# Kernel tuning notes

Hardware: AMD Instinct MI355X
Metric: run time of the kernel (lower is better)

The kernel has to match this reference:

```python
import jax, jax.numpy as jnp
import numpy as np

WIDTH = 1024
NH = 16
HD = 64
MBS = 16
B = 4
L = 2048
BASE_LR = 1.0
EPS = 1e-6


def gelu_tanh(x):
    return jax.nn.gelu(x, approximate=True)


def gelu_bwd(x):
    t = jnp.tanh(0.79788456 * x * (1 + 0.044715 * x * x))
    return 0.5 * x * ((1 - t * t) * (0.79788456 + 0.1070322243 * x * x)) + 0.5 * (1 + t)


def ln_fwd(x, g, b):
    mu = x.mean(-1, keepdims=True)
    var = ((x - mu) ** 2).mean(-1, keepdims=True)
    return g * ((x - mu) * jax.lax.rsqrt(var + EPS)) + b


def ln_l2_bwd(x, tgt, g, b):
    # grad of 0.5*||LN(x)-tgt||^2 wrt x
    mu = x.mean(-1, keepdims=True)
    var = ((x - mu) ** 2).mean(-1, keepdims=True)
    std = jnp.sqrt(var + EPS)
    xh = (x - mu) / std
    gx = (g * xh + b - tgt) * g
    return (gx - gx.mean(-1, keepdims=True) - xh * (gx * xh).mean(-1, keepdims=True)) / std


def adapter_forward(hidden_states, Wq, Wk, Wv, Wo, Wg, lr_w, lr_b,
                    learnable_token_idx, norm_w, norm_b, W1, b1, W2, b2,
                    post_w, post_b):
    Bb, Ll, width = hidden_states.shape
    nh, hd = norm_w.shape
    mbs = learnable_token_idx.shape[0]
    nc = Ll // mbs  # L chosen divisible by mini_batch_size

    def split_heads(x):  # [B,L,width] -> [B,nh,nc,mbs,hd]
        return x.reshape(Bb, Ll, nh, hd).transpose(0, 2, 1, 3).reshape(Bb, nh, nc, mbs, hd)

    XQ = split_heads(hidden_states @ Wq.T)
    XK = split_heads(hidden_states @ Wk.T)
    XV = split_heads(hidden_states @ Wv.T)

    # eta: learnable per-token lr gate (get_eta)
    X = hidden_states.reshape(Bb, nc, mbs, width)
    lr = jnp.einsum('bnkc,hdc->bhnkd', X, lr_w) + lr_b.reshape(1, nh, 1, 1, 1)
    lr = jax.nn.sigmoid(lr).transpose(0, 1, 2, 4, 3)  # [B,nh,nc,1,mbs]
    lr_eta = BASE_LR * lr / hd
    token_idx = jnp.clip(1.0 / jnp.arange(1, mbs + 1, dtype=hidden_states.dtype)
                         + learnable_token_idx, 0.0, None)
    token_eta = token_idx.reshape(1, 1, 1, mbs, 1)
    eta = token_eta * lr_eta  # [B,nh,nc,mbs,mbs]

    tril = jnp.tril(jnp.ones((mbs, mbs), dtype=hidden_states.dtype))
    lnw = norm_w.reshape(nh, 1, hd)
    lnb = norm_b.reshape(nh, 1, hd)

    def step(carry, xs):
        W1s, b1s, W2s, b2s = carry  # [B,nh,hd,4hd], [B,nh,1,4hd], [B,nh,4hd,hd], [B,nh,1,hd]
        XQm, XKm, XVm, etam = xs    # [B,nh,mbs,hd] x3, [B,nh,mbs,mbs]
        X1 = XKm
        Z1 = X1 @ W1s + b1s
        X2 = gelu_tanh(Z1)
        Z2 = X2 @ W2s + b2s
        gZ2 = ln_l2_bwd(Z2, XVm - XKm, lnw, lnb)
        gZ1 = (gZ2 @ jnp.swapaxes(W2s, -1, -2)) * gelu_bwd(Z1)
        eta_tril = etam * tril
        Attn1 = tril * (XQm @ jnp.swapaxes(X1, -1, -2))
        b1_bar = b1s - eta_tril @ gZ1
        Z1_bar = XQm @ W1s - (etam * Attn1) @ gZ1 + b1_bar
        X2_bar = gelu_tanh(Z1_bar)
        Attn2 = tril * (X2_bar @ jnp.swapaxes(X2, -1, -2))
        b2_bar = b2s - eta_tril @ gZ2
        Z2_bar = X2_bar @ W2s - (etam * Attn2) @ gZ2 + b2_bar
        last = etam[:, :, -1, :, None]  # [B,nh,mbs,1]
        W1n = W1s - jnp.swapaxes(last * X1, -1, -2) @ gZ1
        b1n = b1s - (last * gZ1).sum(-2, keepdims=True)
        W2n = W2s - jnp.swapaxes(last * X2, -1, -2) @ gZ2
        b2n = b2s - (last * gZ2).sum(-2, keepdims=True)
        XQW = XQm + ln_fwd(Z2_bar, lnw, lnb)
        return (W1n, b1n, W2n, b2n), XQW

    carry0 = (jnp.broadcast_to(W1, (Bb,) + W1.shape),
              jnp.broadcast_to(b1, (Bb,) + b1.shape),
              jnp.broadcast_to(W2, (Bb,) + W2.shape),
              jnp.broadcast_to(b2, (Bb,) + b2.shape))
    xs = tuple(jnp.moveaxis(t, 2, 0) for t in (XQ, XK, XV, eta))
    _, XQW = jax.lax.scan(step, carry0, xs)  # [nc,B,nh,mbs,hd]
    out = XQW.transpose(1, 0, 3, 2, 4).reshape(Bb, Ll, width)

    # post_norm (LayerNorm eps=1e-6)
    out = ln_fwd(out, post_w, post_b)
    # gate
    out = gelu_tanh(hidden_states @ Wg.T) * out
    # o_proj
    return out @ Wo.T


def setup_inputs():
    key = jax.random.key(0)
    ks = jax.random.split(key, 10)
    n = lambda k, s: jax.random.normal(k, s, dtype=jnp.float32) * 0.02
    return {
        'hidden_states': jax.random.normal(ks[0], (B, L, WIDTH), dtype=jnp.float32),
        'Wq': n(ks[1], (WIDTH, WIDTH)),
        'Wk': n(ks[2], (WIDTH, WIDTH)),
        'Wv': n(ks[3], (WIDTH, WIDTH)),
        'Wo': n(ks[4], (WIDTH, WIDTH)),
        'Wg': n(ks[5], (WIDTH, WIDTH)),
        'lr_w': n(ks[6], (NH, 1, WIDTH)),
        'lr_b': jnp.zeros((NH, 1), jnp.float32),
        'learnable_token_idx': jnp.zeros((MBS,), jnp.float32),
        'norm_w': jnp.ones((NH, HD), jnp.float32),
        'norm_b': jnp.zeros((NH, HD), jnp.float32),
        'W1': n(ks[7], (NH, HD, 4 * HD)),
        'b1': jnp.zeros((NH, 1, 4 * HD), jnp.float32),
        'W2': n(ks[8], (NH, 4 * HD, HD)),
        'b2': jnp.zeros((NH, 1, HD), jnp.float32),
        'post_w': jnp.ones((WIDTH,), jnp.float32),
        'post_b': jnp.zeros((WIDTH,), jnp.float32),
    }


def reference(hidden_states, Wq, Wk, Wv, Wo, Wg, lr_w, lr_b, learnable_token_idx,
              norm_w, norm_b, W1, b1, W2, b2, post_w, post_b):
    return adapter_forward(hidden_states, Wq, Wk, Wv, Wo, Wg, lr_w, lr_b,
                           learnable_token_idx, norm_w, norm_b, W1, b1, W2, b2,
                           post_w, post_b)
```

## Files before the change

### kernel.cpp

```cpp
#include <hip/hip_runtime.h>

#define WIDTH 1024
#define MBSZ 16
#define LLL 2048
#define NCHUNK 128

typedef __attribute__((ext_vector_type(4))) float f32x4;
typedef __attribute__((ext_vector_type(2))) float f32x2;
typedef __attribute__((ext_vector_type(8))) short short8;
typedef __attribute__((ext_vector_type(4))) short short4v;
typedef __attribute__((ext_vector_type(2))) unsigned u32x2;
typedef __attribute__((ext_vector_type(4))) unsigned u32x4;

#define MFMA16(a, b, c) __builtin_amdgcn_mfma_f32_16x16x32_bf16((a), (b), (c), 0, 0, 0)

__device__ __forceinline__ short f2bf(float f) {
  unsigned u = __float_as_uint(f);
  u = (u + 0x7FFFu + ((u >> 16) & 1u)) >> 16;
  return (short)u;
}
__device__ __forceinline__ float bf2f(short s) {
  return __uint_as_float(((unsigned)(unsigned short)s) << 16);
}
__device__ __forceinline__ unsigned cvt_pk(float lo, float hi) {
  unsigned r;
  asm("v_cvt_pk_bf16_f32 %0, %1, %2" : "=v"(r) : "v"(lo), "v"(hi));
  return r;
}
__device__ __forceinline__ float fast_e2u(float x) {
  return __builtin_amdgcn_exp2f(x * (2.30220776f + 0.10294322f * x * x));
}
__device__ __forceinline__ float gelu_f(float x) {
  float e = fast_e2u(x);
  return x * (1.0f - __builtin_amdgcn_rcpf(e + 1.0f));
}
__device__ __forceinline__ float gelu_bwd_f(float x) {
  float e = fast_e2u(x);
  float r = __builtin_amdgcn_rcpf(e + 1.0f);
  return 2.0f * x * r * (1.0f - r) * (0.79788456f + 0.1070322243f * x * x) + (1.0f - r);
}
__device__ __forceinline__ int w2row(int d) { return d * 264 + (d >> 3) * 24; }

__global__ __launch_bounds__(256) void cvt_kernel(const float* __restrict__ hs,
                                                  const float* __restrict__ Wq,
                                                  const float* __restrict__ Wk,
                                                  const float* __restrict__ Wv,
                                                  const float* __restrict__ Wg,
                                                  const float* __restrict__ Wo,
                                                  short* __restrict__ dst) {
  const long idx = ((long)blockIdx.x * 256 + threadIdx.x) * 8;
  if (idx >= 13631488L) return;
  const float* src;
  long off;
  if (idx < 8388608L)       { src = hs; off = idx; }
  else if (idx < 9437184L)  { src = Wq; off = idx - 8388608L; }
  else if (idx < 10485760L) { src = Wk; off = idx - 9437184L; }
  else if (idx < 11534336L) { src = Wv; off = idx - 10485760L; }
  else if (idx < 12582912L) { src = Wg; off = idx - 11534336L; }
  else                      { src = Wo; off = idx - 12582912L; }
  const f32x4 a = *(const f32x4*)(src + off);
  const f32x4 b = *(const f32x4*)(src + off + 4);
  u32x4 o;
  o[0] = cvt_pk(a[0], a[1]); o[1] = cvt_pk(a[2], a[3]);
  o[2] = cvt_pk(b[0], b[1]); o[3] = cvt_pk(b[2], b[3]);
  *(u32x4*)(dst + idx) = o;
}

template <int OUTBF>
__global__ __launch_bounds__(256) void gemm_bt_b(const short* __restrict__ A,
                                                 const short* __restrict__ W,
                                                 float* __restrict__ C,
                                                 short* __restrict__ Cb) {
  __shared__ __align__(16) short sA[64][40];
  __shared__ __align__(16) short sB[64][40];
  const int tid = threadIdx.x;
  const int m0 = blockIdx.x * 64, n0 = blockIdx.y * 64;
  const int srow = tid >> 2, sk = (tid & 3) * 8;
  const int wv = tid >> 6, ln = tid & 63;
  const int fr = ln & 15, kh = (ln >> 4) * 8;
  f32x4 acc[4];
#pragma unroll
  for (int s = 0; s < 4; ++s) acc[s] = (f32x4){0.f, 0.f, 0.f, 0.f};
  const short* ga = A + (long)(m0 + srow) * 1024 + sk;
  const short* gw = W + (long)(n0 + srow) * 1024 + sk;
  for (int k0 = 0; k0 < 1024; k0 += 32) {
    const short8 a8 = *(const short8*)(ga + k0);
    const short8 w8 = *(const short8*)(gw + k0);
    *(short8*)&sA[srow][sk] = a8;
    *(short8*)&sB[srow][sk] = w8;
    __syncthreads();
    short8 af = *(const short8*)&sA[wv * 16 + fr][kh];
#pragma unroll
    for (int s = 0; s < 4; ++s) {
      short8 bf8 = *(const short8*)&sB[s * 16 + fr][kh];
      acc[s] = MFMA16(af, bf8, acc[s]);
    }
    __syncthreads();
  }
  const int orow = m0 + wv * 16 + (ln >> 4) * 4;
#pragma unroll
  for (int s = 0; s < 4; ++s)
#pragma unroll
    for (int q = 0; q < 4; ++q) {
      if (OUTBF)
        Cb[(long)(orow + q) * 1024 + n0 + s * 16 + fr] = f2bf(acc[s][q]);
      else
        C[(long)(orow + q) * 1024 + n0 + s * 16 + fr] = acc[s][q];
    }
}

__global__ __launch_bounds__(256) void lr_kernel(const float* __restrict__ hs,
                                                 const float* __restrict__ lrw,
                                                 const float* __restrict__ lrb,
                                                 float* __restrict__ out) {
  __shared__ __align__(16) float row[1024];
  const int t = blockIdx.x, tid = threadIdx.x;
  *(f32x4*)&row[tid * 4] = *(const f32x4*)&hs[(long)t * 1024 + tid * 4];
  __syncthreads();
  const int hh = tid >> 4, j = tid & 15;
  const float* wrow = lrw + hh * 1024;
  float s = 0.f;
#pragma unroll 4
  for (int m = 0; m < 16; ++m) {
    const int c = j * 4 + m * 64;
    f32x4 x = *(const f32x4*)&row[c];
    f32x4 w = *(const f32x4*)&wrow[c];
    s += x[0] * w[0] + x[1] * w[1] + x[2] * w[2] + x[3] * w[3];
  }
#pragma unroll
  for (int o = 8; o; o >>= 1) s += __shfl_xor(s, o, 16);
  if (j == 0) {
    const float v = s + lrb[hh];
    const float sg = 1.f / (1.f + expf(-v));
    const int b = t >> 11, tr = t & 2047;
    out[((b << 4) + hh) * 2048 + tr] = sg * (1.f / 64.f);
  }
}

__global__ __launch_bounds__(512, 2) void scan_kernel(
    float* __restrict__ Qb, const float* __restrict__ Kb, const float* __restrict__ Vb,
    const float* __restrict__ LRb, const float* __restrict__ lti,
    const float* __restrict__ nw, const float* __restrict__ nb,
    const float* __restrict__ W1in, const float* __restrict__ b1in,
    const float* __restrict__ W2in, const float* __restrict__ b2in) {
  __shared__ __align__(16) short sW1b[256 * 72];
  __shared__ __align__(16) short sW2dp[64 * 264 + 192];
  __shared__ __align__(16) short la1T[64 * 24];
  __shared__ __align__(16) short la2T[256 * 24];
  __shared__ __align__(16) short sX1b[16 * 72];
  __shared__ __align__(16) short sXQb[16 * 72];
  __shared__ __align__(16) float sXQf[16 * 68];
  __shared__ __align__(16) float sTg[16 * 72];
  __shared__ __align__(16) short sX2b[16 * 264];
  __shared__ __align__(16) short sXbb[16 * 264];
  __shared__ __align__(16) short sG1c[256 * 24];
  __shared__ __align__(16) short sG2b[16 * 72];
  __shared__ __align__(16) short sG2c[64 * 24];
  __shared__ __align__(16) float sZ2f[16 * 68];
  __shared__ __align__(16) short sC1b[16 * 24];
  __shared__ __align__(16) short sC2b[16 * 24];
  __shared__ __align__(16) float sB1[256];
  __shared__ __align__(16) float sB2[64];
  __shared__ float sLr[16];
  __shared__ float sTok[16];
  __shared__ __align__(16) float sLnw[64];
  __shared__ __align__(16) float sLnb[64];

  const int bh = blockIdx.x, b = bh >> 4, h = bh & 15;
  const int tid = threadIdx.x;
  const int w = tid >> 6, ln = tid & 63;
  const int fr = ln & 15, half = ln >> 4, hk = half * 8;
  const int nt0 = 2 * w;

  float w1m[8][4], w2m[8][4];
#pragma unroll
  for (int r = 0; r < 8; ++r) {
    const int T = w * 8 + r, dt = T >> 4, pt = T & 15;
#pragma unroll
    for (int qq = 0; qq < 4; ++qq) {
      w1m[r][qq] = W1in[h * 16384 + (dt * 16 + half * 4 + qq) * 256 + pt * 16 + fr];
      w2m[r][qq] = W2in[h * 16384 + (pt * 16 + half * 4 + qq) * 64 + dt * 16 + fr];
    }
  }
  for (int e = tid; e < 16384; e += 512) {
    {
      const int d = e >> 8, p = e & 255;
      sW1b[p * 72 + d] = f2bf(W1in[h * 16384 + e]);
    }
    {
      const int p = e >> 6, d = e & 63;
      sW2dp[w2row(d) + (p ^ (((d >> 3) & 3) << 3))] = f2bf(W2in[h * 16384 + e]);
    }
  }
  if (tid < 256) sB1[tid] = b1in[h * 256 + tid];
  if (tid < 64) { sB2[tid] = b2in[h * 64 + tid]; sLnw[tid] = nw[h * 64 + tid]; sLnb[tid] = nb[h * 64 + tid]; }
  if (tid < 16) sTok[tid] = fmaxf(1.0f / (float)(tid + 1) + lti[tid], 0.0f);

  const f32x4 zf4 = (f32x4){0.f, 0.f, 0.f, 0.f};
  short8 zs8;
#pragma unroll
  for (int j = 0; j < 8; ++j) zs8[j] = 0;

  const int pf_i = tid >> 5;
  const int pf_d = (tid & 31) * 2;
  f32x2 pk, pq, pv;
  float plr = 0.f;
  {
    const long a0 = ((long)(b * LLL + pf_i)) * WIDTH + h * 64 + pf_d;
    pk = *(const f32x2*)&Kb[a0];
    pq = *(const f32x2*)&Qb[a0];
    pv = *(const f32x2*)&Vb[a0];
    if (tid < 16) plr = LRb[(long)bh * 2048 + tid];
  }

  for (int n = 0; n < NCHUNK; ++n) {
    const long gbase = ((long)(b * LLL + n * MBSZ)) * WIDTH + h * 64;

    {
      *(unsigned*)&sX1b[pf_i * 72 + pf_d] = cvt_pk(pk[0], pk[1]);
      *(unsigned*)&sXQb[pf_i * 72 + pf_d] = cvt_pk(pq[0], pq[1]);
      sXQf[pf_i * 68 + pf_d] = pq[0];
      sXQf[pf_i * 68 + pf_d + 1] = pq[1];
      sTg[pf_i * 72 + pf_d] = pv[0] - pk[0];
      sTg[pf_i * 72 + pf_d + 1] = pv[1] - pk[1];
      if (tid < 16) sLr[tid] = plr;
    }
    __syncthreads();

    short8 aX1[2], aXQ[2];
    aX1[0] = *(const short8*)&sX1b[fr * 72 + hk];
    aX1[1] = *(const short8*)&sX1b[fr * 72 + 32 + hk];
    aXQ[0] = *(const short8*)&sXQb[fr * 72 + hk];
    aXQ[1] = *(const short8*)&sXQb[fr * 72 + 32 + hk];
    f32x4 z1[2], q1[2];
    float b1p[2];
#pragma unroll
    for (int t = 0; t < 2; ++t) {
      const int p = (nt0 + t) * 16 + fr;
      z1[t] = zf4; q1[t] = zf4;
#pragma unroll
      for (int ks = 0; ks < 2; ++ks) {
        short8 bw = *(const short8*)&sW1b[p * 72 + ks * 32 + hk];
        z1[t] = MFMA16(aX1[ks], bw, z1[t]);
        q1[t] = MFMA16(aXQ[ks], bw, q1[t]);
      }
      b1p[t] = sB1[p];
#pragma unroll
      for (int qq = 0; qq < 4; ++qq) {
        z1[t][qq] += b1p[t];
        sX2b[(half * 4 + qq) * 264 + p] = f2bf(gelu_f(z1[t][qq]));
      }
    }
    {
      const float tok15 = sTok[15];
      const int d = tid >> 3, j0 = (tid & 7) * 2;
      const float v0 = bf2f(sX1b[j0 * 72 + d]) * (tok15 * sLr[j0]);
      const float v1 = bf2f(sX1b[(j0 + 1) * 72 + d]) * (tok15 * sLr[j0 + 1]);
      *(unsigned*)&la1T[d * 24 + j0] = cvt_pk(v0, v1);
    }
    if (w == 0) {
      f32x4 c = MFMA16(aXQ[0], aX1[0], zf4);
      c = MFMA16(aXQ[1], aX1[1], c);
#pragma unroll
      for (int qq = 0; qq < 4; ++qq) {
        const int i = half * 4 + qq, j = fr;
        sC1b[i * 24 + j] = f2bf((i >= j) ? sTok[i] * sLr[j] * (c[qq] + 1.0f) : 0.0f);
      }
    }
    __syncthreads();

    float bb2old = 0.f;
    if (w < 4) {
      const int d = w * 16 + fr;
      const int sw = ((d >> 3) & 3) << 3;
      const int rb = w2row(d);
      f32x4 za = zf4, zb = zf4;
#pragma unroll
      for (int ks = 0; ks < 4; ++ks) {
        short8 a = *(const short8*)&sX2b[fr * 264 + ks * 32 + hk];
        short8 bfr = *(const short8*)&sW2dp[rb + ((ks * 32 + hk) ^ sw)];
        za = MFMA16(a, bfr, za);
      }
#pragma unroll
      for (int ks = 4; ks < 8; ++ks) {
        short8 a = *(const short8*)&sX2b[fr * 264 + ks * 32 + hk];
        short8 bfr = *(const short8*)&sW2dp[rb + ((ks * 32 + hk) ^ sw)];
        zb = MFMA16(a, bfr, zb);
      }
      bb2old = sB2[d];
#pragma unroll
      for (int qq = 0; qq < 4; ++qq)
        sZ2f[(half * 4 + qq) * 68 + d] = za[qq] + zb[qq] + bb2old;
    }
    __syncthreads();

    if (tid < 256) {
      const int i = tid >> 4, j4 = tid & 15;
      const f32x4 z = *(const f32x4*)&sZ2f[i * 68 + j4 * 4];
      float s1 = z[0] + z[1] + z[2] + z[3];
      float s2 = z[0] * z[0] + z[1] * z[1] + z[2] * z[2] + z[3] * z[3];
#pragma unroll
      for (int o = 8; o; o >>= 1) { s1 += __shfl_xor(s1, o, 16); s2 += __shfl_xor(s2, o, 16); }
      const float mu = s1 * (1.f / 64.f);
      const float rstd = rsqrtf(s2 * (1.f / 64.f) - mu * mu + 1e-6f);
      const f32x4 g = *(const f32x4*)&sLnw[j4 * 4];
      const f32x4 bb = *(const f32x4*)&sLnb[j4 * 4];
      const f32x4 tg = *(const f32x4*)&sTg[i * 72 + j4 * 4];
      f32x4 xh, gx;
      float a1 = 0.f, a2 = 0.f;
#pragma unroll
      for (int e = 0; e < 4; ++e) {
        xh[e] = (z[e] - mu) * rstd;
        gx[e] = (g[e] * xh[e] + bb[e] - tg[e]) * g[e];
        a1 += gx[e]; a2 += gx[e] * xh[e];
      }
#pragma unroll
      for (int o = 8; o; o >>= 1) { a1 += __shfl_xor(a1, o, 16); a2 += __shfl_xor(a2, o, 16); }
      const float m1 = a1 * (1.f / 64.f), m2 = a2 * (1.f / 64.f);
      float o4[4];
#pragma unroll
      for (int e = 0; e < 4; ++e) o4[e] = (gx[e] - m1 - xh[e] * m2) * rstd;
      const unsigned lo = cvt_pk(o4[0], o4[1]);
      const unsigned hi = cvt_pk(o4[2], o4[3]);
      *(u32x2*)&sG2b[i * 72 + j4 * 4] = (u32x2){lo, hi};
      sG2c[(j4 * 4 + 0) * 24 + i] = (short)lo;
      sG2c[(j4 * 4 + 1) * 24 + i] = (short)(lo >> 16);
      sG2c[(j4 * 4 + 2) * 24 + i] = (short)hi;
      sG2c[(j4 * 4 + 3) * 24 + i] = (short)(hi >> 16);
    } else {
      const int pp = tid - 256;
      const float tok15 = sTok[15];
      unsigned uu[8];
#pragma unroll
      for (int jp = 0; jp < 8; ++jp) {
        const float v0 = bf2f(sX2b[(2 * jp) * 264 + pp]) * (tok15 * sLr[2 * jp]);
        const float v1 = bf2f(sX2b[(2 * jp + 1) * 264 + pp]) * (tok15 * sLr[2 * jp + 1]);
        uu[jp] = cvt_pk(v0, v1);
      }
      *(u32x4*)&la2T[pp * 24] = (u32x4){uu[0], uu[1], uu[2], uu[3]};
      *(u32x4*)&la2T[pp * 24 + 8] = (u32x4){uu[4], uu[5], uu[6], uu[7]};
    }
    __syncthreads();

    {
      short8 aG2[2];
      aG2[0] = *(const short8*)&sG2b[fr * 72 + hk];
      aG2[1] = *(const short8*)&sG2b[fr * 72 + 32 + hk];
#pragma unroll
      for (int t = 0; t < 2; ++t) {
        const int p = (nt0 + t) * 16 + fr;
        f32x4 g = zf4;
#pragma unroll
        for (int ks = 0; ks < 2; ++ks) {
          const int dg = ks * 32 + hk;
          const int rb = w2row(dg) + (p ^ (((dg >> 3) & 3) << 3));
          short8 bw;
#pragma unroll
          for (int jj = 0; jj < 8; ++jj) bw[jj] = sW2dp[rb + jj * 264];
          g = MFMA16(aG2[ks], bw, g);
        }
        const unsigned lo = cvt_pk(g[0] * gelu_bwd_f(z1[t][0]), g[1] * gelu_bwd_f(z1[t][1]));
        const unsigned hi = cvt_pk(g[2] * gelu_bwd_f(z1[t][2]), g[3] * gelu_bwd_f(z1[t][3]));
        *(u32x2*)&sG1c[p * 24 + half * 4] = (u32x2){lo, hi};
      }
    }
    if (tid < 64) {
      float s = 0.f;
#pragma unroll
      for (int j = 0; j < 16; ++j) s += sLr[j] * bf2f(sG2c[tid * 24 + j]);
      sB2[tid] -= sTok[15] * s;
    }
    __syncthreads();

    {
      short8 ac = zs8;
      if (half < 2) ac = *(const short8*)&sC1b[fr * 24 + hk];
#pragma unroll
      for (int t = 0; t < 2; ++t) {
        const int p = (nt0 + t) * 16 + fr;
        short8 bg = zs8;
        if (half < 2) bg = *(const short8*)&sG1c[p * 24 + hk];
        f32x4 corr = MFMA16(ac, bg, zf4);
#pragma unroll
        for (int qq = 0; qq < 4; ++qq)
          sXbb[(half * 4 + qq) * 264 + p] = f2bf(gelu_f(q1[t][qq] + b1p[t] - corr[qq]));
      }
    }
    {
#pragma unroll
      for (int r = 0; r < 8; ++r) {
        const int T = w * 8 + r, dt = T >> 4, pt = T & 15;
        short8 af = zs8, bg = zs8;
        if (half < 2) {
          af = *(const short8*)&la1T[(dt * 16 + fr) * 24 + hk];
          bg = *(const short8*)&sG1c[(pt * 16 + fr) * 24 + hk];
        }
        f32x4 dl = MFMA16(af, bg, zf4);
        const int pp = pt * 16 + fr, d0 = dt * 16 + half * 4;
        w1m[r][0] -= dl[0]; w1m[r][1] -= dl[1]; w1m[r][2] -= dl[2]; w1m[r][3] -= dl[3];
        const unsigned lo = cvt_pk(w1m[r][0], w1m[r][1]);
        const unsigned hi = cvt_pk(w1m[r][2], w1m[r][3]);
        *(u32x2*)&sW1b[pp * 72 + d0] = (u32x2){lo, hi};
      }
    }
    if (tid < 256) {
      float s = 0.f;
#pragma unroll
      for (int j = 0; j < 16; ++j) s += sLr[j] * bf2f(sG1c[tid * 24 + j]);
      sB1[tid] -= sTok[15] * s;
    }
    __syncthreads();

    {
      const int nn = (n + 1 < NCHUNK) ? n + 1 : n;
      const long a1 = ((long)(b * LLL + nn * MBSZ + pf_i)) * WIDTH + h * 64 + pf_d;
      pk = *(const f32x2*)&Kb[a1];
      pq = *(const f32x2*)&Qb[a1];
      pv = *(const f32x2*)&Vb[a1];
      if (tid < 16) plr = LRb[(long)bh * 2048 + nn * MBSZ + tid];
    }
    f32x4 zbar = zf4;
    if (w < 4) {
      const int d = w * 16 + fr;
      const int sw = ((d >> 3) & 3) << 3;
      const int rb = w2row(d);
      f32x4 za = zf4, zb = zf4;
#pragma unroll
      for (int ks = 0; ks < 4; ++ks) {
        short8 a = *(const short8*)&sXbb[fr * 264 + ks * 32 + hk];
        short8 bfr = *(const short8*)&sW2dp[rb + ((ks * 32 + hk) ^ sw)];
        za = MFMA16(a, bfr, za);
      }
#pragma unroll
      for (int ks = 4; ks < 8; ++ks) {
        short8 a = *(const short8*)&sXbb[fr * 264 + ks * 32 + hk];
        short8 bfr = *(const short8*)&sW2dp[rb + ((ks * 32 + hk) ^ sw)];
        zb = MFMA16(a, bfr, zb);
      }
      zbar[0] = za[0] + zb[0]; zbar[1] = za[1] + zb[1];
      zbar[2] = za[2] + zb[2]; zbar[3] = za[3] + zb[3];
    } else if (w == 4) {
      f32x4 c = zf4;
#pragma unroll
      for (int ks = 0; ks < 8; ++ks) {
        short8 a = *(const short8*)&sXbb[fr * 264 + ks * 32 + hk];
        short8 bx = *(const short8*)&sX2b[fr * 264 + ks * 32 + hk];
        c = MFMA16(a, bx, c);
      }
#pragma unroll
      for (int qq = 0; qq < 4; ++qq) {
        const int i = half * 4 + qq, j = fr;
        sC2b[i * 24 + j] = f2bf((i >= j) ? sTok[i] * sLr[j] * (c[qq] + 1.0f) : 0.0f);
      }
    }
    __syncthreads();

    if (w < 4) {
      const int d = w * 16 + fr;
      short8 ac = zs8, bg = zs8;
      if (half < 2) {
        ac = *(const short8*)&sC2b[fr * 24 + hk];
        bg = *(const short8*)&sG2c[d * 24 + hk];
      }
      f32x4 corr = MFMA16(ac, bg, zf4);
#pragma unroll
      for (int qq = 0; qq < 4; ++qq)
        sZ2f[(half * 4 + qq) * 68 + d] = zbar[qq] + bb2old - corr[qq];
    }
    {
#pragma unroll
      for (int r = 0; r < 8; ++r) {
        const int T = w * 8 + r, pt = T & 15, dt = T >> 4;
        short8 af = zs8, bg = zs8;
        if (half < 2) {
          af = *(const short8*)&la2T[(pt * 16 + fr) * 24 + hk];
          bg = *(const short8*)&sG2c[(dt * 16 + fr) * 24 + hk];
        }
        f32x4 dl = MFMA16(af, bg, zf4);
        const int dd = dt * 16 + fr;
        const int swp = ((dd >> 3) & 3) << 3;
        const int p0 = pt * 16 + half * 4;
        w2m[r][0] -= dl[0]; w2m[r][1] -= dl[1]; w2m[r][2] -= dl[2]; w2m[r][3] -= dl[3];
        const unsigned lo = cvt_pk(w2m[r][0], w2m[r][1]);
        const unsigned hi = cvt_pk(w2m[r][2], w2m[r][3]);
        *(u32x2*)&sW2dp[w2row(dd) + (p0 ^ swp)] = (u32x2){lo, hi};
      }
    }
    __syncthreads();

    if (tid < 256) {
      const int i = tid >> 4, j4 = tid & 15;
      const f32x4 z = *(const f32x4*)&sZ2f[i * 68 + j4 * 4];
      float s1 = z[0] + z[1] + z[2] + z[3];
      float s2 = z[0] * z[0] + z[1] * z[1] + z[2] * z[2] + z[3] * z[3];
#pragma unroll
      for (int o = 8; o; o >>= 1) { s1 += __shfl_xor(s1, o, 16); s2 += __shfl_xor(s2, o, 16); }
      const float mu = s1 * (1.f / 64.f);
      const float rstd = rsqrtf(s2 * (1.f / 64.f) - mu * mu + 1e-6f);
      const f32x4 g = *(const f32x4*)&sLnw[j4 * 4];
      const f32x4 bb = *(const f32x4*)&sLnb[j4 * 4];
      const f32x4 xq = *(const f32x4*)&sXQf[i * 68 + j4 * 4];
      f32x4 o4;
#pragma unroll
      for (int e = 0; e < 4; ++e) o4[e] = xq[e] + g[e] * ((z[e] - mu) * rstd) + bb[e];
      *(f32x4*)&Qb[gbase + (long)i * WIDTH + j4 * 4] = o4;
    }
    __syncthreads();
  }
}

__global__ __launch_bounds__(256) void epi_kernel(const float* __restrict__ X,
                                                  const short* __restrict__ G,
                                                  const float* __restrict__ pw,
                                                  const float* __restrict__ pb,
                                                  short* __restrict__ T) {
  __shared__ float red[8];
  const int t = blockIdx.x, tid = threadIdx.x;
  const long base = (long)t * 1024 + tid * 4;
  f32x4 x = *(const f32x4*)&X[base];
  float s1 = x[0] + x[1] + x[2] + x[3];
  float s2 = x[0] * x[0] + x[1] * x[1] + x[2] * x[2] + x[3] * x[3];
#pragma unroll
  for (int o = 32; o; o >>= 1) { s1 += __shfl_xor(s1, o, 64); s2 += __shfl_xor(s2, o, 64); }
  const int wv = tid >> 6, ln = tid & 63;
  if (ln == 0) { red[wv] = s1; red[4 + wv] = s2; }
  __syncthreads();
  s1 = red[0] + red[1] + red[2] + red[3];
  s2 = red[4] + red[5] + red[6] + red[7];
  const float mu = s1 * (1.f / 1024.f);
  const float rstd = rsqrtf(s2 * (1.f / 1024.f) - mu * mu + 1e-6f);
  const short4v g4 = *(const short4v*)&G[base];
  f32x4 w = *(const f32x4*)&pw[tid * 4];
  f32x4 bb = *(const f32x4*)&pb[tid * 4];
  float o4[4];
#pragma unroll
  for (int e = 0; e < 4; ++e) {
    float y = w[e] * ((x[e] - mu) * rstd) + bb[e];
    o4[e] = gelu_f(bf2f(g4[e])) * y;
  }
  *(u32x2*)&T[base] = (u32x2){cvt_pk(o4[0], o4[1]), cvt_pk(o4[2], o4[3])};
}

extern "C" void kernel_launch(void* const* d_in, const int* in_sizes, int n_in,
                              void* d_out, int out_size, void* d_ws, size_t ws_size,
                              hipStream_t stream) {
  const float* hs  = (const float*)d_in[0];
  const float* Wq  = (const float*)d_in[1];
  const float* Wk  = (const float*)d_in[2];
  const float* Wv  = (const float*)d_in[3];
  const float* Wo  = (const float*)d_in[4];
  const float* Wg  = (const float*)d_in[5];
  const float* lrw = (const float*)d_in[6];
  const float* lrb = (const float*)d_in[7];
  const float* lti = (const float*)d_in[8];
  const float* nw  = (const float*)d_in[9];
  const float* nb  = (const float*)d_in[10];
  const float* W1  = (const float*)d_in[11];
  const float* b1  = (const float*)d_in[12];
  const float* W2  = (const float*)d_in[13];
  const float* b2  = (const float*)d_in[14];
  const float* pw  = (const float*)d_in[15];
  const float* pb  = (const float*)d_in[16];
  float* out = (float*)d_out;
  float* ws = (float*)d_ws;

  float* Qb  = ws;
  float* Kb  = ws + 8388608;
  float* Vb  = ws + 16777216;
  float* LRb = ws + 25165824;
  short* hsb = (short*)(ws + 25296896);
  short* Wqb = hsb + 8388608;
  short* Wkb = Wqb + 1048576;
  short* Wvb = Wkb + 1048576;
  short* Wgb = Wvb + 1048576;
  short* Wob = Wgb + 1048576;
  short* Tb  = (short*)Kb;
  short* Gbb = (short*)Vb;

  dim3 gg(128, 16);
  cvt_kernel<<<6656, 256, 0, stream>>>(hs, Wq, Wk, Wv, Wg, Wo, hsb);
  gemm_bt_b<0><<<gg, 256, 0, stream>>>(hsb, Wqb, Qb, nullptr);
  gemm_bt_b<0><<<gg, 256, 0, stream>>>(hsb, Wkb, Kb, nullptr);
  gemm_bt_b<0><<<gg, 256, 0, stream>>>(hsb, Wvb, Vb, nullptr);
  lr_kernel<<<8192, 256, 0, stream>>>(hs, lrw, lrb, LRb);
  scan_kernel<<<64, 512, 0, stream>>>(Qb, Kb, Vb, LRb, lti, nw, nb, W1, b1, W2, b2);
  gemm_bt_b<1><<<gg, 256, 0, stream>>>(hsb, Wgb, nullptr, Gbb);
  epi_kernel<<<8192, 256, 0, stream>>>(Qb, Gbb, pw, pb, Tb);
  gemm_bt_b<0><<<gg, 256, 0, stream>>>(Tb, Wob, out, nullptr);
}
```

Before: 990.9 us.

## Overlap gate GEMM with sequential scan and merge QKV/lr kernels

```diff
diff --git a/kernel.cpp b/kernel.cpp
--- a/kernel.cpp
+++ b/kernel.cpp
@@ -66,11 +66,9 @@
   *(u32x4*)(dst + idx) = o;
 }
 
-template <int OUTBF>
 __global__ __launch_bounds__(256) void gemm_bt_b(const short* __restrict__ A,
                                                  const short* __restrict__ W,
-                                                 float* __restrict__ C,
-                                                 short* __restrict__ Cb) {
+                                                 float* __restrict__ C) {
   __shared__ __align__(16) short sA[64][40];
   __shared__ __align__(16) short sB[64][40];
   const int tid = threadIdx.x;
@@ -101,48 +99,92 @@
 #pragma unroll
   for (int s = 0; s < 4; ++s)
 #pragma unroll
-    for (int q = 0; q < 4; ++q) {
-      if (OUTBF)
-        Cb[(long)(orow + q) * 1024 + n0 + s * 16 + fr] = f2bf(acc[s][q]);
-      else
+    for (int q = 0; q < 4; ++q)
+      C[(long)(orow + q) * 1024 + n0 + s * 16 + fr] = acc[s][q];
+}
+
+__global__ __launch_bounds__(256) void qkv_lr_kernel(const short* __restrict__ hsb,
+                                                     const short* __restrict__ Wqb,
+                                                     const short* __restrict__ Wkb,
+                                                     const short* __restrict__ Wvb,
+                                                     float* __restrict__ Qb,
+                                                     float* __restrict__ Kb,
+                                                     float* __restrict__ Vb,
+                                                     const float* __restrict__ hs,
+                                                     const float* __restrict__ lrw,
+                                                     const float* __restrict__ lrb,
+                                                     float* __restrict__ LRb) {
+  __shared__ __align__(16) short sA[64][40];
+  __shared__ __align__(16) short sB[64][40];
+  __shared__ __align__(16) float row[1024];
+  const int tid = threadIdx.x;
+  const int idx = blockIdx.x;
+  if (idx < 6144) {
+    const int which = idx >> 11, t = idx & 2047;
+    const int m0 = (t & 127) * 64, n0 = (t >> 7) * 64;
+    const short* W = (which == 0) ? Wqb : (which == 1) ? Wkb : Wvb;
+    float* C = (which == 0) ? Qb : (which == 1) ? Kb : Vb;
+    const int srow = tid >> 2, sk = (tid & 3) * 8;
+    const int wv = tid >> 6, ln = tid & 63;
+    const int fr = ln & 15, kh = (ln >> 4) * 8;
+    f32x4 acc[4];
+#pragma unroll
+    for (int s = 0; s < 4; ++s) acc[s] = (f32x4){0.f, 0.f, 0.f, 0.f};
+    const short* ga = hsb + (long)(m0 + srow) * 1024 + sk;
+    const short* gw = W + (long)(n0 + srow) * 1024 + sk;
+    for (int k0 = 0; k0 < 1024; k0 += 32) {
+      const short8 a8 = *(const short8*)(ga + k0);
+      const short8 w8 = *(const short8*)(gw + k0);
+      *(short8*)&sA[srow][sk] = a8;
+      *(short8*)&sB[srow][sk] = w8;
+      __syncthreads();
+      short8 af = *(const short8*)&sA[wv * 16 + fr][kh];
+#pragma unroll
+      for (int s = 0; s < 4; ++s) {
+        short8 bf8 = *(const short8*)&sB[s * 16 + fr][kh];
+        acc[s] = MFMA16(af, bf8, acc[s]);
+      }
+      __syncthreads();
+    }
+    const int orow = m0 + wv * 16 + (ln >> 4) * 4;
+#pragma unroll
+    for (int s = 0; s < 4; ++s)
+#pragma unroll
+      for (int q = 0; q < 4; ++q)
         C[(long)(orow + q) * 1024 + n0 + s * 16 + fr] = acc[s][q];
-    }
-}
-
-__global__ __launch_bounds__(256) void lr_kernel(const float* __restrict__ hs,
-                                                 const float* __restrict__ lrw,
-                                                 const float* __restrict__ lrb,
-                                                 float* __restrict__ out) {
-  __shared__ __align__(16) float row[1024];
-  const int t = blockIdx.x, tid = threadIdx.x;
-  *(f32x4*)&row[tid * 4] = *(const f32x4*)&hs[(long)t * 1024 + tid * 4];
-  __syncthreads();
-  const int hh = tid >> 4, j = tid & 15;
-  const float* wrow = lrw + hh * 1024;
-  float s = 0.f;
+  } else {
+    const int t = idx - 6144;
+    *(f32x4*)&row[tid * 4] = *(const f32x4*)&hs[(long)t * 1024 + tid * 4];
+    __syncthreads();
+    const int hh = tid >> 4, j = tid & 15;
+    const float* wrow = lrw + hh * 1024;
+    float s = 0.f;
 #pragma unroll 4
-  for (int m = 0; m < 16; ++m) {
-    const int c = j * 4 + m * 64;
-    f32x4 x = *(const f32x4*)&row[c];
-    f32x4 w = *(const f32x4*)&wrow[c];
-    s += x[0] * w[0] + x[1] * w[1] + x[2] * w[2] + x[3] * w[3];
-  }
-#pragma unroll
-  for (int o = 8; o; o >>= 1) s += __shfl_xor(s, o, 16);
-  if (j == 0) {
-    const float v = s + lrb[hh];
-    const float sg = 1.f / (1.f + expf(-v));
-    const int b = t >> 11, tr = t & 2047;
-    out[((b << 4) + hh) * 2048 + tr] = sg * (1.f / 64.f);
-  }
-}
-
-__global__ __launch_bounds__(512, 2) void scan_kernel(
+    for (int m = 0; m < 16; ++m) {
+      const int c = j * 4 + m * 64;
+      f32x4 x = *(const f32x4*)&row[c];
+      f32x4 w = *(const f32x4*)&wrow[c];
+      s += x[0] * w[0] + x[1] * w[1] + x[2] * w[2] + x[3] * w[3];
+    }
+#pragma unroll
+    for (int o = 8; o; o >>= 1) s += __shfl_xor(s, o, 16);
+    if (j == 0) {
+      const float v = s + lrb[hh];
+      const float sg = 1.f / (1.f + expf(-v));
+      const int b = t >> 11, tr = t & 2047;
+      LRb[((b << 4) + hh) * 2048 + tr] = sg * (1.f / 64.f);
+    }
+  }
+}
+
+__global__ __launch_bounds__(512, 2) void scan_gate_kernel(
     float* __restrict__ Qb, const float* __restrict__ Kb, const float* __restrict__ Vb,
     const float* __restrict__ LRb, const float* __restrict__ lti,
     const float* __restrict__ nw, const float* __restrict__ nb,
     const float* __restrict__ W1in, const float* __restrict__ b1in,
-    const float* __restrict__ W2in, const float* __restrict__ b2in) {
+    const float* __restrict__ W2in, const float* __restrict__ b2in,
+    const short* __restrict__ hsA, const short* __restrict__ Wgb,
+    short* __restrict__ Gout) {
   __shared__ __align__(16) short sW1b[256 * 72];
   __shared__ __align__(16) short sW2dp[64 * 264 + 192];
   __shared__ __align__(16) short la1T[64 * 24];
@@ -166,8 +208,46 @@
   __shared__ __align__(16) float sLnw[64];
   __shared__ __align__(16) float sLnb[64];
 
+  const int tid = threadIdx.x;
+
+  if (blockIdx.x >= 64) {
+    const int hh = tid >> 8, t2 = tid & 255;
+    const int tile = (blockIdx.x - 64) * 2 + hh;
+    const int m0 = (tile & 127) * 64, n0 = (tile >> 7) * 64;
+    short* sAh = sW1b + hh * 2560;
+    short* sBh = sW1b + 5120 + hh * 2560;
+    const int srow = t2 >> 2, sk = (t2 & 3) * 8;
+    const int wv2 = t2 >> 6, ln2 = t2 & 63;
+    const int fr2 = ln2 & 15, kh2 = (ln2 >> 4) * 8;
+    f32x4 acc[4];
+#pragma unroll
+    for (int s = 0; s < 4; ++s) acc[s] = (f32x4){0.f, 0.f, 0.f, 0.f};
+    const short* ga = hsA + (long)(m0 + srow) * 1024 + sk;
+    const short* gw = Wgb + (long)(n0 + srow) * 1024 + sk;
+    for (int k0 = 0; k0 < 1024; k0 += 32) {
+      const short8 a8 = *(const short8*)(ga + k0);
+      const short8 w8 = *(const short8*)(gw + k0);
+      *(short8*)&sAh[srow * 40 + sk] = a8;
+      *(short8*)&sBh[srow * 40 + sk] = w8;
+      __syncthreads();
+      short8 af = *(const short8*)&sAh[(wv2 * 16 + fr2) * 40 + kh2];
+#pragma unroll
+      for (int s = 0; s < 4; ++s) {
+        short8 bf8 = *(const short8*)&sBh[(s * 16 + fr2) * 40 + kh2];
+        acc[s] = MFMA16(af, bf8, acc[s]);
+      }
+      __syncthreads();
+    }
+    const int orow = m0 + wv2 * 16 + (ln2 >> 4) * 4;
+#pragma unroll
+    for (int s = 0; s < 4; ++s)
+#pragma unroll
+      for (int q = 0; q < 4; ++q)
+        Gout[(long)(orow + q) * 1024 + n0 + s * 16 + fr2] = f2bf(acc[s][q]);
+    return;
+  }
+
   const int bh = blockIdx.x, b = bh >> 4, h = bh & 15;
-  const int tid = threadIdx.x;
   const int w = tid >> 6, ln = tid & 63;
   const int fr = ln & 15, half = ln >> 4, hk = half * 8;
   const int nt0 = 2 * w;
@@ -353,10 +433,10 @@
 #pragma unroll
         for (int ks = 0; ks < 2; ++ks) {
           const int dg = ks * 32 + hk;
-          const int rb = w2row(dg) + (p ^ (((dg >> 3) & 3) << 3));
+          const int rb2 = w2row(dg) + (p ^ (((dg >> 3) & 3) << 3));
           short8 bw;
 #pragma unroll
-          for (int jj = 0; jj < 8; ++jj) bw[jj] = sW2dp[rb + jj * 264];
+          for (int jj = 0; jj < 8; ++jj) bw[jj] = sW2dp[rb2 + jj * 264];
           g = MFMA16(aG2[ks], bw, g);
         }
         const unsigned lo = cvt_pk(g[0] * gelu_bwd_f(z1[t][0]), g[1] * gelu_bwd_f(z1[t][1]));
@@ -367,7 +447,12 @@
     if (tid < 64) {
       float s = 0.f;
 #pragma unroll
-      for (int j = 0; j < 16; ++j) s += sLr[j] * bf2f(sG2c[tid * 24 + j]);
+      for (int k = 0; k < 4; ++k) {
+        const short4v g4 = *(const short4v*)&sG2c[tid * 24 + k * 4];
+        const f32x4 lr4 = *(const f32x4*)&sLr[k * 4];
+        s += lr4[0] * bf2f(g4[0]) + lr4[1] * bf2f(g4[1]) +
+             lr4[2] * bf2f(g4[2]) + lr4[3] * bf2f(g4[3]);
+      }
       sB2[tid] -= sTok[15] * s;
     }
     __syncthreads();
@@ -406,7 +491,12 @@
     if (tid < 256) {
       float s = 0.f;
 #pragma unroll
-      for (int j = 0; j < 16; ++j) s += sLr[j] * bf2f(sG1c[tid * 24 + j]);
+      for (int k = 0; k < 4; ++k) {
+        const short4v g4 = *(const short4v*)&sG1c[tid * 24 + k * 4];
+        const f32x4 lr4 = *(const f32x4*)&sLr[k * 4];
+        s += lr4[0] * bf2f(g4[0]) + lr4[1] * bf2f(g4[1]) +
+             lr4[2] * bf2f(g4[2]) + lr4[3] * bf2f(g4[3]);
+      }
       sB1[tid] -= sTok[15] * s;
     }
     __syncthreads();
@@ -575,16 +665,12 @@
   short* Wgb = Wvb + 1048576;
   short* Wob = Wgb + 1048576;
   short* Tb  = (short*)Kb;
-  short* Gbb = (short*)Vb;
-
-  dim3 gg(128, 16);
+  short* Gbb = (short*)out;
+
   cvt_kernel<<<6656, 256, 0, stream>>>(hs, Wq, Wk, Wv, Wg, Wo, hsb);
-  gemm_bt_b<0><<<gg, 256, 0, stream>>>(hsb, Wqb, Qb, nullptr);
-  gemm_bt_b<0><<<gg, 256, 0, stream>>>(hsb, Wkb, Kb, nullptr);
-  gemm_bt_b<0><<<gg, 256, 0, stream>>>(hsb, Wvb, Vb, nullptr);
-  lr_kernel<<<8192, 256, 0, stream>>>(hs, lrw, lrb, LRb);
-  scan_kernel<<<64, 512, 0, stream>>>(Qb, Kb, Vb, LRb, lti, nw, nb, W1, b1, W2, b2);
-  gemm_bt_b<1><<<gg, 256, 0, stream>>>(hsb, Wgb, nullptr, Gbb);
+  qkv_lr_kernel<<<14336, 256, 0, stream>>>(hsb, Wqb, Wkb, Wvb, Qb, Kb, Vb, hs, lrw, lrb, LRb);
+  scan_gate_kernel<<<1088, 512, 0, stream>>>(Qb, Kb, Vb, LRb, lti, nw, nb, W1, b1, W2, b2,
+                                             hsb, Wgb, Gbb);
   epi_kernel<<<8192, 256, 0, stream>>>(Qb, Gbb, pw, pb, Tb);
-  gemm_bt_b<0><<<gg, 256, 0, stream>>>(Tb, Wob, out, nullptr);
-}
+  gemm_bt_b<<<dim3(128, 16), 256, 0, stream>>>(Tb, Wob, out);
+}
```

After: 945.2 us. -4.6%, faster.
